# Optimization experiments

Hardware: AMD Instinct MI355X
Metric: run time of the kernel (lower is better)

The kernel has to match this reference:

```python
import jax, jax.numpy as jnp
import numpy as np

N_NODES = 50000
N_EDGES = 800000
IN_FEAT = 128
HIDDEN = 128
HEADS = 4
HEAD_DIM = HIDDEN // HEADS  # 32
N_LAYERS = 3
N_GRAPHS = 64
NEG_SLOPE = 0.2
LN_EPS = 1e-5


def setup_inputs() -> dict:
    key = jax.random.key(0)
    ks = jax.random.split(key, 12)
    x = jax.random.normal(ks[0], (N_NODES, IN_FEAT), dtype=jnp.float32)
    edge_index = jax.random.randint(ks[1], (2, N_EDGES), 0, N_NODES, dtype=jnp.int64)
    batch = jnp.sort(jax.random.randint(ks[2], (N_NODES,), 0, N_GRAPHS, dtype=jnp.int64))
    s = 0.05
    emb_W = jax.random.normal(ks[3], (IN_FEAT, HIDDEN), dtype=jnp.float32) * s
    emb_b = jnp.zeros((HIDDEN,), dtype=jnp.float32)
    lin_l_W = jax.random.normal(ks[4], (N_LAYERS, HIDDEN, HIDDEN), dtype=jnp.float32) * s
    lin_l_b = jnp.zeros((N_LAYERS, HIDDEN), dtype=jnp.float32)
    lin_r_W = jax.random.normal(ks[5], (N_LAYERS, HIDDEN, HIDDEN), dtype=jnp.float32) * s
    lin_r_b = jnp.zeros((N_LAYERS, HIDDEN), dtype=jnp.float32)
    att = jax.random.normal(ks[6], (N_LAYERS, HEADS, HEAD_DIM), dtype=jnp.float32) * s
    conv_b = jnp.zeros((N_LAYERS, HIDDEN), dtype=jnp.float32)
    ln_g = jnp.ones((N_LAYERS, HIDDEN), dtype=jnp.float32)
    ln_b = jnp.zeros((N_LAYERS, HIDDEN), dtype=jnp.float32)
    return {"x": x, "edge_index": edge_index, "batch": batch,
            "emb_W": emb_W, "emb_b": emb_b,
            "lin_l_W": lin_l_W, "lin_l_b": lin_l_b,
            "lin_r_W": lin_r_W, "lin_r_b": lin_r_b,
            "att": att, "conv_b": conv_b, "ln_g": ln_g, "ln_b": ln_b}


def _gatv2_layer(x, src, dst, Wl, bl, Wr, br, att_w, bias):
    # x: [N, HIDDEN]; src/dst: [E]; att_w: [H, C]
    N = x.shape[0]
    xl = (x @ Wl + bl).reshape(N, HEADS, HEAD_DIM)  # source transform
    xr = (x @ Wr + br).reshape(N, HEADS, HEAD_DIM)  # target transform
    e = jax.nn.leaky_relu(xl[src] + xr[dst], NEG_SLOPE)      # [E, H, C]
    logits = jnp.einsum('ehc,hc->eh', e, att_w)              # [E, H]
    # segment softmax over edges grouped by destination node
    seg_max = jax.ops.segment_max(logits, dst, num_segments=N)  # [N, H]
    seg_max = jnp.where(jnp.isfinite(seg_max), seg_max, 0.0)
    ex = jnp.exp(logits - seg_max[dst])
    denom = jax.ops.segment_sum(ex, dst, num_segments=N)
    alpha = ex / (denom[dst] + 1e-16)                        # [E, H]
    msg = alpha[..., None] * xl[src]                         # [E, H, C]
    out = jax.ops.segment_sum(msg, dst, num_segments=N)      # [N, H, C]
    return out.reshape(N, HIDDEN) + bias


def _layer_norm(x, g, b):
    mu = jnp.mean(x, axis=-1, keepdims=True)
    var = jnp.mean(jnp.square(x - mu), axis=-1, keepdims=True)
    return (x - mu) * jax.lax.rsqrt(var + LN_EPS) * g + b


def reference(x, edge_index, batch, emb_W, emb_b, lin_l_W, lin_l_b,
              lin_r_W, lin_r_b, att, conv_b, ln_g, ln_b):
    src, dst = edge_index[0], edge_index[1]
    h = x @ emb_W + emb_b
    for l in range(N_LAYERS):
        res = h
        h = _gatv2_layer(h, src, dst, lin_l_W[l], lin_l_b[l],
                         lin_r_W[l], lin_r_b[l], att[l], conv_b[l])
        h = jax.nn.elu(h)          # dropout in eval mode = identity
        h = h + res
        h = _layer_norm(h, ln_g[l], ln_b[l])
    # global mean pool over graphs
    sums = jax.ops.segment_sum(h, batch, num_segments=N_GRAPHS)
    counts = jax.ops.segment_sum(jnp.ones((h.shape[0], 1), h.dtype), batch,
                                 num_segments=N_GRAPHS)
    return sums / jnp.maximum(counts, 1.0)
```

## Files before the change

### kernel.cpp

```cpp
#include <hip/hip_runtime.h>
#include <hip/hip_bf16.h>
#include <math.h>


#define HID 128
#define BKT_SHIFT 7
#define BKT_DSTS (1 << BKT_SHIFT)
#define CAP_SHIFT 12
#define CAP (1 << CAP_SHIFT)

typedef __attribute__((ext_vector_type(8))) short bf8_t;
typedef __attribute__((ext_vector_type(8))) _Float16 hf8_t;
typedef __attribute__((ext_vector_type(2))) _Float16 h2_t;
typedef __attribute__((ext_vector_type(4))) float f4_t;

__device__ __forceinline__ unsigned short f2bf(float f) {
    unsigned u = __float_as_uint(f);
    u += 0x7fff + ((u >> 16) & 1);
    return (unsigned short)(u >> 16);
}
__device__ __forceinline__ float bf2f(unsigned short h) {
    return __uint_as_float(((unsigned)h) << 16);
}
__device__ __forceinline__ unsigned short f2h(float f) {
    _Float16 h = (_Float16)f;
    return __builtin_bit_cast(unsigned short, h);
}
__device__ __forceinline__ float h2f(unsigned short u) {
    return (float)__builtin_bit_cast(_Float16, u);
}
__device__ __forceinline__ h2_t shfl_xor_h2(h2_t v, int m) {
    return __builtin_bit_cast(h2_t, __shfl_xor(__builtin_bit_cast(int, v), m, 64));
}


__global__ __launch_bounds__(256) void k1_bin_prep(
    const int* __restrict__ ei, int* __restrict__ bucketCursor,
    int* __restrict__ tmp, int E, int NBK, int perBlk,
    const float* __restrict__ embW, const float* __restrict__ linlW,
    const float* __restrict__ linrW, unsigned short* __restrict__ frag) {
    __shared__ int hist[512];
    __shared__ int base[512];
    int tid = threadIdx.x;

    if (blockIdx.x < 256) {
        int e0 = blockIdx.x * perBlk;
        int e1 = e0 + perBlk; if (e1 > E) e1 = E;

        for (int b = tid; b < NBK; b += 256) hist[b] = 0;
        __syncthreads();
        for (int e = e0 + tid; e < e1; e += 256)
            atomicAdd(&hist[ei[E + e] >> BKT_SHIFT], 1);
        __syncthreads();
        for (int b = tid; b < NBK; b += 256) {
            int c = hist[b];
            if (c > 0) base[b] = atomicAdd(&bucketCursor[b], c);
            hist[b] = 0;
        }
        __syncthreads();
        for (int e = e0 + tid; e < e1; e += 256) {
            int d = ei[E + e];
            int b = d >> BKT_SHIFT;
            int pos = (b << CAP_SHIFT) + base[b] + atomicAdd(&hist[b], 1);
            tmp[pos] = ei[e] | ((d & (BKT_DSTS - 1)) << 16);
        }
    } else {
        int bid = blockIdx.x - 256;
        int w = bid >> 6;
        const float* W;
        if (w == 0)      W = embW;
        else if (w <= 3) W = linlW + (size_t)(w - 1) * 16384;
        else             W = linrW + (size_t)(w - 4) * 16384;

        int i = ((bid & 63) << 8) + tid;
        int j = i & 7;
        int lane = (i >> 3) & 63;
        int t = i >> 9;
        int kk = t >> 3, nn = t & 7;
        int k = kk * 32 + (lane >> 4) * 8 + j;
        int n = nn * 16 + (lane & 15);
        float v = W[k * 128 + n];
        if (w == 0) {
            unsigned short hi = f2bf(v);
            frag[i] = hi;
            frag[16384 + i] = f2bf(v - bf2f(hi));
        } else {
            int slot = (w <= 3) ? (1 + 2 * (w - 1)) : (2 + 2 * (w - 4));
            frag[32768 + (size_t)(slot - 1) * 16384 + i] = f2h(v);
        }
    }
}


__global__ __launch_bounds__(256) void k2_bucket_embdual(
    const int* __restrict__ tmp, const int* __restrict__ bucketCursor,
    int* __restrict__ offsets, int* __restrict__ deg,
    unsigned short* __restrict__ srt, int N, int GBLK,
    const float* __restrict__ Afp, const unsigned short* __restrict__ wfrag,
    const float* __restrict__ emb_b,
    const float* __restrict__ bl0, const float* __restrict__ br0,
    unsigned short* __restrict__ Chi, unsigned short* __restrict__ Clo,
    unsigned short* __restrict__ xl, unsigned short* __restrict__ xr) {
    __shared__ __align__(16) unsigned short As[2][64][136];
    int tid = threadIdx.x;

    if (blockIdx.x >= GBLK) {
        int* hist = (int*)As;
        int* cur  = hist + BKT_DSTS;
        int b = blockIdx.x - GBLK;
        int d0 = b << BKT_SHIFT;
        if (tid < BKT_DSTS) hist[tid] = 0;
        __syncthreads();
        int start = b << CAP_SHIFT;
        int end = start + bucketCursor[b];
        for (int i = start + tid; i < end; i += 256)
            atomicAdd(&hist[(tmp[i] >> 16) & (BKT_DSTS - 1)], 1);
        __syncthreads();
        int v = (tid < BKT_DSTS) ? hist[tid] : 0;
        if (tid < BKT_DSTS) cur[tid] = v;
        __syncthreads();
        for (int off = 1; off < BKT_DSTS; off <<= 1) {
            int u = (tid < BKT_DSTS && tid >= off) ? cur[tid - off] : 0;
            __syncthreads();
            if (tid < BKT_DSTS) cur[tid] += u;
            __syncthreads();
        }
        if (tid < BKT_DSTS) {
            int ex = start + cur[tid] - v;
            int d = d0 + tid;
            if (d < N) { offsets[d] = ex; deg[d] = v; }
            cur[tid] = ex;
        }
        __syncthreads();
        for (int i = start + tid; i < end; i += 256) {
            int r = tmp[i];
            int pos = atomicAdd(&cur[(r >> 16) & (BKT_DSTS - 1)], 1);
            srt[pos] = (unsigned short)(r & 0xFFFF);
        }
        return;
    }

    int m0 = blockIdx.x * 64;

    #pragma unroll
    for (int i = 0; i < 8; ++i) {
        int idx = tid + i * 256;
        int r = idx >> 5, c4 = idx & 31;
        int row = m0 + r;
        float4 v = make_float4(0.f, 0.f, 0.f, 0.f);
        if (row < N) v = *(const float4*)(Afp + (size_t)row * HID + c4 * 4);
        ushort4 hi, lo;
        hi.x = f2bf(v.x); lo.x = f2bf(v.x - bf2f(hi.x));
        hi.y = f2bf(v.y); lo.y = f2bf(v.y - bf2f(hi.y));
        hi.z = f2bf(v.z); lo.z = f2bf(v.z - bf2f(hi.z));
        hi.w = f2bf(v.w); lo.w = f2bf(v.w - bf2f(hi.w));
        *(ushort4*)&As[0][r][c4 * 4] = hi;
        *(ushort4*)&As[1][r][c4 * 4] = lo;
    }
    __syncthreads();

    int wave = tid >> 6, lane = tid & 63;
    int mrow = lane & 15;
    int quad = lane >> 4;

    f4_t acc[8];
    #pragma unroll
    for (int nn = 0; nn < 8; ++nn) acc[nn] = (f4_t)(0.f);

    #pragma unroll
    for (int kk = 0; kk < 4; ++kk) {
        bf8_t ah = *(const bf8_t*)&As[0][wave * 16 + mrow][kk * 32 + quad * 8];
        bf8_t al = *(const bf8_t*)&As[1][wave * 16 + mrow][kk * 32 + quad * 8];
        const unsigned short* bp = wfrag + kk * 4096 + lane * 8;
        #pragma unroll
        for (int nn = 0; nn < 8; ++nn) {
            bf8_t bh = *(const bf8_t*)(bp + nn * 512);
            bf8_t bl = *(const bf8_t*)(bp + nn * 512 + 16384);
            acc[nn] = __builtin_amdgcn_mfma_f32_16x16x32_bf16(ah, bh, acc[nn], 0, 0, 0);
            acc[nn] = __builtin_amdgcn_mfma_f32_16x16x32_bf16(ah, bl, acc[nn], 0, 0, 0);
            acc[nn] = __builtin_amdgcn_mfma_f32_16x16x32_bf16(al, bh, acc[nn], 0, 0, 0);
        }
    }

    int lrow0 = wave * 16 + quad * 4;
    __syncthreads();
    #pragma unroll
    for (int nn = 0; nn < 8; ++nn) {
        int col = nn * 16 + mrow;
        float b = emb_b[col];
        #pragma unroll
        for (int r = 0; r < 4; ++r) {
            float o = acc[nn][r] + b;
            unsigned short hh = f2h(o);
            As[0][lrow0 + r][col] = hh;
            As[1][lrow0 + r][col] = f2h(o - h2f(hh));
        }
    }
    __syncthreads();

    hf8_t afr[4];
    #pragma unroll
    for (int kk = 0; kk < 4; ++kk)
        afr[kk] = *(const hf8_t*)&As[0][wave * 16 + mrow][kk * 32 + quad * 8];
    #pragma unroll
    for (int i = 0; i < 4; ++i) {
        int idx = tid + i * 256;
        int r = idx >> 4, c8 = idx & 15;
        int row = m0 + r;
        if (row < N) {
            *(uint4*)(Chi + (size_t)row * HID + c8 * 8) = *(uint4*)&As[0][r][c8 * 8];
            *(uint4*)(Clo + (size_t)row * HID + c8 * 8) = *(uint4*)&As[1][r][c8 * 8];
        }
    }

    f4_t acc0[8], acc1[8];
    #pragma unroll
    for (int nn = 0; nn < 8; ++nn) {
        acc0[nn] = (f4_t)(0.f);
        acc1[nn] = (f4_t)(0.f);
    }
    const unsigned short* Bl = wfrag + 32768;
    const unsigned short* Br = wfrag + 49152;
    #pragma unroll
    for (int kk = 0; kk < 4; ++kk) {
        const unsigned short* bp0 = Bl + kk * 4096 + lane * 8;
        const unsigned short* bp1 = Br + kk * 4096 + lane * 8;
        #pragma unroll
        for (int nn = 0; nn < 8; ++nn) {
            hf8_t bb0 = *(const hf8_t*)(bp0 + nn * 512);
            hf8_t bb1 = *(const hf8_t*)(bp1 + nn * 512);
            acc0[nn] = __builtin_amdgcn_mfma_f32_16x16x32_f16(afr[kk], bb0, acc0[nn], 0, 0, 0);
            acc1[nn] = __builtin_amdgcn_mfma_f32_16x16x32_f16(afr[kk], bb1, acc1[nn], 0, 0, 0);
        }
    }

    __syncthreads();
    #pragma unroll
    for (int nn = 0; nn < 8; ++nn) {
        int col = nn * 16 + mrow;
        float bb0 = bl0[col];
        float bb1 = br0[col];
        #pragma unroll
        for (int r = 0; r < 4; ++r) {
            As[0][lrow0 + r][col] = f2h(acc0[nn][r] + bb0);
            As[1][lrow0 + r][col] = f2h(acc1[nn][r] + bb1);
        }
    }
    __syncthreads();
    #pragma unroll
    for (int i = 0; i < 4; ++i) {
        int idx = tid + i * 256;
        int r = idx >> 4, c8 = idx & 15;
        int row = m0 + r;
        if (row < N) {
            *(uint4*)(xl + (size_t)row * HID + c8 * 8) = *(uint4*)&As[0][r][c8 * 8];
            *(uint4*)(xr + (size_t)row * HID + c8 * 8) = *(uint4*)&As[1][r][c8 * 8];
        }
    }
}


__global__ __launch_bounds__(256) void gemm_dual_f16(
    const unsigned short* __restrict__ Ah,
    const unsigned short* __restrict__ Bf0, const unsigned short* __restrict__ Bf1,
    const float* __restrict__ b0, const float* __restrict__ b1,
    unsigned short* __restrict__ C0h, unsigned short* __restrict__ C1h, int M) {
    __shared__ __align__(16) unsigned short As[2][64][136];
    int m0 = blockIdx.x * 64;
    int tid = threadIdx.x;

    #pragma unroll
    for (int i = 0; i < 4; ++i) {
        int idx = tid + i * 256;
        int r = idx >> 4, c8 = idx & 15;
        int row = m0 + r;
        uint4 v = make_uint4(0, 0, 0, 0);
        if (row < M) v = *(const uint4*)(Ah + (size_t)row * HID + c8 * 8);
        *(uint4*)&As[0][r][c8 * 8] = v;
    }
    __syncthreads();

    int wave = tid >> 6, lane = tid & 63;
    int mrow = lane & 15;
    int quad = lane >> 4;

    f4_t acc0[8], acc1[8];
    #pragma unroll
    for (int nn = 0; nn < 8; ++nn) {
        acc0[nn] = (f4_t)(0.f);
        acc1[nn] = (f4_t)(0.f);
    }

    #pragma unroll
    for (int kk = 0; kk < 4; ++kk) {
        hf8_t a = *(const hf8_t*)&As[0][wave * 16 + mrow][kk * 32 + quad * 8];
        const unsigned short* bp0 = Bf0 + kk * 4096 + lane * 8;
        const unsigned short* bp1 = Bf1 + kk * 4096 + lane * 8;
        #pragma unroll
        for (int nn = 0; nn < 8; ++nn) {
            hf8_t bb0 = *(const hf8_t*)(bp0 + nn * 512);
            hf8_t bb1 = *(const hf8_t*)(bp1 + nn * 512);
            acc0[nn] = __builtin_amdgcn_mfma_f32_16x16x32_f16(a, bb0, acc0[nn], 0, 0, 0);
            acc1[nn] = __builtin_amdgcn_mfma_f32_16x16x32_f16(a, bb1, acc1[nn], 0, 0, 0);
        }
    }

    int lrow0 = wave * 16 + quad * 4;
    __syncthreads();
    #pragma unroll
    for (int nn = 0; nn < 8; ++nn) {
        int col = nn * 16 + mrow;
        float bb0 = b0[col];
        float bb1 = b1[col];
        #pragma unroll
        for (int r = 0; r < 4; ++r) {
            As[0][lrow0 + r][col] = f2h(acc0[nn][r] + bb0);
            As[1][lrow0 + r][col] = f2h(acc1[nn][r] + bb1);
        }
    }
    __syncthreads();
    #pragma unroll
    for (int i = 0; i < 4; ++i) {
        int idx = tid + i * 256;
        int r = idx >> 4, c8 = idx & 15;
        int row = m0 + r;
        if (row < M) {
            *(uint4*)(C0h + (size_t)row * HID + c8 * 8) = *(uint4*)&As[0][r][c8 * 8];
            *(uint4*)(C1h + (size_t)row * HID + c8 * 8) = *(uint4*)&As[1][r][c8 * 8];
        }
    }
}


__device__ __forceinline__ void edge_math(uint4 rv, const h2_t xr2[4], const h2_t av2[4],
                                          h2_t xv[4], float* pOut) {
    const h2_t slope2 = {(_Float16)0.2f, (_Float16)0.2f};
    xv[0] = __builtin_bit_cast(h2_t, rv.x); xv[1] = __builtin_bit_cast(h2_t, rv.y);
    xv[2] = __builtin_bit_cast(h2_t, rv.z); xv[3] = __builtin_bit_cast(h2_t, rv.w);
    h2_t p2 = (h2_t)((_Float16)0.f);
    #pragma unroll
    for (int i = 0; i < 4; ++i) {
        h2_t e = xv[i] + xr2[i];
        e = __builtin_elementwise_max(e, e * slope2);
        p2 = e * av2[i] + p2;
    }
    *pOut = (float)p2[0] + (float)p2[1];
}

__global__ __launch_bounds__(256) void gat_layer(
    const unsigned short* __restrict__ xlh,
    const unsigned short* __restrict__ xrh,
    const int* __restrict__ offsets, const int* __restrict__ deg,
    const unsigned short* __restrict__ srt,
    const float* __restrict__ att,
    const float* __restrict__ convb,
    const float* __restrict__ lng, const float* __restrict__ lnb,
    unsigned short* __restrict__ Hhi, unsigned short* __restrict__ Hlo, int N) {
    int wv = (blockIdx.x * blockDim.x + threadIdx.x) >> 6;
    int lane = threadIdx.x & 63;
    if (wv >= N) return;
    int n = wv;
    int quarter = lane >> 4;
    int f0 = (lane & 15) * 8;
    const unsigned short* xbase = xlh + f0;

    h2_t xr2[4], av2[4];
    {
        uint4 xv = *(const uint4*)(xrh + (size_t)n * HID + f0);
        xr2[0] = __builtin_bit_cast(h2_t, xv.x);
        xr2[1] = __builtin_bit_cast(h2_t, xv.y);
        xr2[2] = __builtin_bit_cast(h2_t, xv.z);
        xr2[3] = __builtin_bit_cast(h2_t, xv.w);
        float a[8];
        *(float4*)&a[0] = *(const float4*)(att + f0);
        *(float4*)&a[4] = *(const float4*)(att + f0 + 4);
        #pragma unroll
        for (int i = 0; i < 4; ++i)
            av2[i] = (h2_t){(_Float16)a[2 * i], (_Float16)a[2 * i + 1]};
    }

    float d = 0.f;
    h2_t acc2[4];
    #pragma unroll
    for (int i = 0; i < 4; ++i) acc2[i] = (h2_t)((_Float16)0.f);
    int start = offsets[n], cnt = deg[n];

    int j = 0;
    for (; j + 16 <= cnt; j += 16) {
        int s[4];
        #pragma unroll
        for (int u = 0; u < 4; ++u) s[u] = srt[start + j + 4 * u + quarter];
        uint4 rv[4];
        #pragma unroll
        for (int u = 0; u < 4; ++u)
            rv[u] = *(const uint4*)(xbase + (size_t)s[u] * HID);
        h2_t xv[4][4];
        float p[4];
        #pragma unroll
        for (int u = 0; u < 4; ++u) edge_math(rv[u], xr2, av2, xv[u], &p[u]);
        h2_t p01 = {(_Float16)p[0], (_Float16)p[1]};
        h2_t p23 = {(_Float16)p[2], (_Float16)p[3]};
        p01 += shfl_xor_h2(p01, 1); p23 += shfl_xor_h2(p23, 1);
        p01 += shfl_xor_h2(p01, 2); p23 += shfl_xor_h2(p23, 2);
        float w[4];
        w[0] = __expf((float)p01[0]); w[1] = __expf((float)p01[1]);
        w[2] = __expf((float)p23[0]); w[3] = __expf((float)p23[1]);
        #pragma unroll
        for (int u = 0; u < 4; ++u) {
            d += w[u];
            h2_t w2 = (h2_t)((_Float16)w[u]);
            #pragma unroll
            for (int i = 0; i < 4; ++i) acc2[i] = w2 * xv[u][i] + acc2[i];
        }
    }
    for (; j + 4 <= cnt; j += 4) {
        int s = srt[start + j + quarter];
        uint4 rv = *(const uint4*)(xbase + (size_t)s * HID);
        h2_t xv[4];
        float p;
        edge_math(rv, xr2, av2, xv, &p);
        p += __shfl_xor(p, 1, 64);
        p += __shfl_xor(p, 2, 64);
        float w = __expf(p);
        d += w;
        h2_t w2 = (h2_t)((_Float16)w);
        #pragma unroll
        for (int i = 0; i < 4; ++i) acc2[i] = w2 * xv[i] + acc2[i];
    }
    if (j < cnt) {
        int r = cnt - j;
        int idx = j + quarter; if (idx > cnt - 1) idx = cnt - 1;
        int s = srt[start + idx];
        uint4 rv = *(const uint4*)(xbase + (size_t)s * HID);
        h2_t xv[4];
        float p;
        edge_math(rv, xr2, av2, xv, &p);
        p += __shfl_xor(p, 1, 64);
        p += __shfl_xor(p, 2, 64);
        float w = (quarter < r) ? __expf(p) : 0.f;
        d += w;
        h2_t w2 = (h2_t)((_Float16)w);
        #pragma unroll
        for (int i = 0; i < 4; ++i) acc2[i] = w2 * xv[i] + acc2[i];
    }

    #pragma unroll
    for (int i = 0; i < 4; ++i) {
        acc2[i] += shfl_xor_h2(acc2[i], 16);
        acc2[i] += shfl_xor_h2(acc2[i], 32);
    }
    d += __shfl_xor(d, 16, 64);
    d += __shfl_xor(d, 32, 64);

    float acc[8];
    #pragma unroll
    for (int i = 0; i < 4; ++i) {
        acc[2 * i]     = (float)acc2[i][0];
        acc[2 * i + 1] = (float)acc2[i][1];
    }

    float inv = 1.f / (d + 1e-16f);
    float t[8];
    {
        float cb[8];
        *(float4*)&cb[0] = *(const float4*)(convb + f0);
        *(float4*)&cb[4] = *(const float4*)(convb + f0 + 4);
        uint4 rh = *(const uint4*)(Hhi + (size_t)n * HID + f0);
        uint4 rl = *(const uint4*)(Hlo + (size_t)n * HID + f0);
        const unsigned short* hs = (const unsigned short*)&rh;
        const unsigned short* ls = (const unsigned short*)&rl;
        #pragma unroll
        for (int i = 0; i < 8; ++i) {
            float g = acc[i] * inv + cb[i];
            g = (g > 0.f) ? g : (__expf(g) - 1.f);
            t[i] = g + (h2f(hs[i]) + h2f(ls[i]));
        }
    }

    float sum = 0.f;
    #pragma unroll
    for (int i = 0; i < 8; ++i) sum += t[i];
    #pragma unroll
    for (int m = 1; m <= 8; m <<= 1) sum += __shfl_xor(sum, m, 64);
    float mu = sum * (1.f / 128.f);
    float q[8], vs = 0.f;
    #pragma unroll
    for (int i = 0; i < 8; ++i) { q[i] = t[i] - mu; vs += q[i] * q[i]; }
    #pragma unroll
    for (int m = 1; m <= 8; m <<= 1) vs += __shfl_xor(vs, m, 64);
    float rstd = rsqrtf(vs * (1.f / 128.f) + 1e-5f);

    if (quarter == 0) {
        float gv[8], bv[8], o[8];
        *(float4*)&gv[0] = *(const float4*)(lng + f0);
        *(float4*)&gv[4] = *(const float4*)(lng + f0 + 4);
        *(float4*)&bv[0] = *(const float4*)(lnb + f0);
        *(float4*)&bv[4] = *(const float4*)(lnb + f0 + 4);
        #pragma unroll
        for (int i = 0; i < 8; ++i) o[i] = q[i] * rstd * gv[i] + bv[i];
        unsigned short hh[8], hl[8];
        #pragma unroll
        for (int i = 0; i < 8; ++i) {
            hh[i] = f2h(o[i]);
            hl[i] = f2h(o[i] - h2f(hh[i]));
        }
        *(uint4*)(Hhi + (size_t)n * HID + f0) = *(uint4*)&hh[0];
        *(uint4*)(Hlo + (size_t)n * HID + f0) = *(uint4*)&hl[0];
    }
}


__global__ __launch_bounds__(256) void pool_partial(const unsigned short* __restrict__ Hhi,
                                                    const unsigned short* __restrict__ Hlo,
                                                    const int* __restrict__ batch,
                                                    float* __restrict__ sums, int N) {
    __shared__ int bsh[64];
    int c0 = blockIdx.x * 64;
    int tid = threadIdx.x;
    if (tid < 64) bsh[tid] = (c0 + tid < N) ? batch[c0 + tid] : -1;
    __syncthreads();

    int r = tid >> 5;
    int f0 = (tid & 31) * 4;
    float4 acc = make_float4(0.f, 0.f, 0.f, 0.f);
    int curg = -1;
    #pragma unroll
    for (int i = 0; i < 8; ++i) {
        int li = r * 8 + i;
        int g = bsh[li];
        if (g < 0) break;
        if (g != curg) {
            if (curg >= 0) {
                atomicAdd(&sums[curg * HID + f0 + 0], acc.x);
                atomicAdd(&sums[curg * HID + f0 + 1], acc.y);
                atomicAdd(&sums[curg * HID + f0 + 2], acc.z);
                atomicAdd(&sums[curg * HID + f0 + 3], acc.w);
            }
            acc = make_float4(0.f, 0.f, 0.f, 0.f);
            curg = g;
        }
        size_t base = (size_t)(c0 + li) * HID + f0;
        ushort4 hh = *(const ushort4*)(Hhi + base);
        ushort4 hl = *(const ushort4*)(Hlo + base);
        acc.x += h2f(hh.x) + h2f(hl.x);
        acc.y += h2f(hh.y) + h2f(hl.y);
        acc.z += h2f(hh.z) + h2f(hl.z);
        acc.w += h2f(hh.w) + h2f(hl.w);
    }
    if (curg >= 0) {
        atomicAdd(&sums[curg * HID + f0 + 0], acc.x);
        atomicAdd(&sums[curg * HID + f0 + 1], acc.y);
        atomicAdd(&sums[curg * HID + f0 + 2], acc.z);
        atomicAdd(&sums[curg * HID + f0 + 3], acc.w);
    }
}

__global__ __launch_bounds__(128) void pool_final(const float* __restrict__ sums,
                                                  const int* __restrict__ batch,
                                                  float* __restrict__ out, int N) {
    int g = blockIdx.x;
    int f = threadIdx.x;
    int lo = 0, hi = N;
    while (lo < hi) { int mid = (lo + hi) >> 1; if (batch[mid] < g) lo = mid + 1; else hi = mid; }
    int s0 = lo;
    lo = 0; hi = N;
    while (lo < hi) { int mid = (lo + hi) >> 1; if (batch[mid] < g + 1) lo = mid + 1; else hi = mid; }
    int cnt = lo - s0; if (cnt < 1) cnt = 1;
    out[g * HID + f] = sums[g * HID + f] / (float)cnt;
}


extern "C" void kernel_launch(void* const* d_in, const int* in_sizes, int n_in,
                              void* d_out, int out_size, void* d_ws, size_t ws_size,
                              hipStream_t stream) {
    const float* x      = (const float*)d_in[0];
    const int*   ei     = (const int*)d_in[1];
    const int*   batch  = (const int*)d_in[2];
    const float* emb_W  = (const float*)d_in[3];
    const float* emb_b  = (const float*)d_in[4];
    const float* linlW  = (const float*)d_in[5];
    const float* linlb  = (const float*)d_in[6];
    const float* linrW  = (const float*)d_in[7];
    const float* linrb  = (const float*)d_in[8];
    const float* att    = (const float*)d_in[9];
    const float* convb  = (const float*)d_in[10];
    const float* lng    = (const float*)d_in[11];
    const float* lnb    = (const float*)d_in[12];
    float* out = (float*)d_out;

    const int N = in_sizes[0] / HID;
    const int E = in_sizes[1] / 2;
    const int NG = out_size / HID;
    const int NBK = (N + BKT_DSTS - 1) / BKT_DSTS;

    char* p = (char*)d_ws;
    unsigned short* xlh = (unsigned short*)p; p += (size_t)N * HID * 2;
    unsigned short* xrh = (unsigned short*)p; p += (size_t)N * HID * 2;
    unsigned short* hhi = (unsigned short*)p; p += (size_t)N * HID * 2;
    unsigned short* hlo = (unsigned short*)p; p += (size_t)N * HID * 2;
    unsigned short* wfrag = (unsigned short*)p; p += (32768 + 6 * 16384) * 2;
    float* sums       = (float*)p; p += (size_t)NG * HID * 4;
    int* bucketCursor = (int*)p; p += (size_t)((NBK + 63) & ~63) * 4;
    int* deg          = (int*)p; p += (size_t)N * 4;
    int* offsets      = (int*)p; p += (size_t)N * 4;
    unsigned short* srt = (unsigned short*)p; p += ((size_t)NBK << CAP_SHIFT) * 2;
    int* tmp          = (int*)p; p += ((size_t)NBK << CAP_SHIFT) * 4;

    size_t zbytes = (size_t)NG * HID * 4 + (size_t)((NBK + 63) & ~63) * 4;
    hipMemsetAsync(sums, 0, zbytes, stream);

    int perBlk = (E + 255) / 256;
    k1_bin_prep<<<256 + 448, 256, 0, stream>>>(ei, bucketCursor, tmp, E, NBK, perBlk,
                                               emb_W, linlW, linrW, wfrag);

    int gblk = (N + 63) / 64;
    k2_bucket_embdual<<<gblk + NBK, 256, 0, stream>>>(tmp, bucketCursor, offsets, deg,
                                                      srt, N, gblk,
                                                      x, wfrag, emb_b, linlb, linrb,
                                                      hhi, hlo, xlh, xrh);

    gat_layer<<<(N + 3) / 4, 256, 0, stream>>>(xlh, xrh, offsets, deg, srt,
                                               att, convb, lng, lnb, hhi, hlo, N);

    for (int l = 1; l < 3; ++l) {
        const unsigned short* wl = wfrag + 32768 + (size_t)(2 * l) * 16384;
        const unsigned short* wr = wfrag + 32768 + (size_t)(2 * l + 1) * 16384;
        gemm_dual_f16<<<gblk, 256, 0, stream>>>(hhi, wl, wr,
                                                linlb + (size_t)l * HID,
                                                linrb + (size_t)l * HID,
                                                xlh, xrh, N);
        gat_layer<<<(N + 3) / 4, 256, 0, stream>>>(xlh, xrh, offsets, deg, srt,
                                                   att + (size_t)l * HID,
                                                   convb + (size_t)l * HID,
                                                   lng + (size_t)l * HID,
                                                   lnb + (size_t)l * HID,
                                                   hhi, hlo, N);
    }

    pool_partial<<<(N + 63) / 64, 256, 0, stream>>>(hhi, hlo, batch, sums, N);
    pool_final<<<NG, 128, 0, stream>>>(sums, batch, out, N);
}
```

Before: 337.3 us.

## Replace bucketed two-pass edge sort with global-atomic count, scan, scatter

Replaces the bucketed counting sort (per-block LDS histograms writing into a packed tmp array, then per-bucket re-sorting) with a direct CSR build. Per-destination degrees are counted with global atomics, each bucket is scanned into offsets, and a new scatter kernel places source indices using per-destination atomic cursors. This drops the intermediate tmp buffer and its extra read/write pass. In exchange it adds a kernel launch, global atomic contention on degree counters, and scattered 2-byte writes, and edge order within a destination becomes nondeterministic.

After: 398.2 us. 1.18x slower.

```diff
diff --git a/kernel.cpp b/kernel.cpp
--- a/kernel.cpp
+++ b/kernel.cpp
@@ -7,7 +7,8 @@
 #define BKT_SHIFT 7
 #define BKT_DSTS (1 << BKT_SHIFT)
 #define CAP_SHIFT 12
-#define CAP (1 << CAP_SHIFT)
+#define CNT_BLOCKS 1024
+#define SCT_BLOCKS 1024
 
 typedef __attribute__((ext_vector_type(8))) short bf8_t;
 typedef __attribute__((ext_vector_type(8))) _Float16 hf8_t;
@@ -34,38 +35,18 @@
 }
 
 
-__global__ __launch_bounds__(256) void k1_bin_prep(
-    const int* __restrict__ ei, int* __restrict__ bucketCursor,
-    int* __restrict__ tmp, int E, int NBK, int perBlk,
+__global__ __launch_bounds__(256) void k1_count_prep(
+    const int* __restrict__ ei, int* __restrict__ deg, int E,
     const float* __restrict__ embW, const float* __restrict__ linlW,
     const float* __restrict__ linrW, unsigned short* __restrict__ frag) {
-    __shared__ int hist[512];
-    __shared__ int base[512];
     int tid = threadIdx.x;
 
-    if (blockIdx.x < 256) {
-        int e0 = blockIdx.x * perBlk;
-        int e1 = e0 + perBlk; if (e1 > E) e1 = E;
-
-        for (int b = tid; b < NBK; b += 256) hist[b] = 0;
-        __syncthreads();
-        for (int e = e0 + tid; e < e1; e += 256)
-            atomicAdd(&hist[ei[E + e] >> BKT_SHIFT], 1);
-        __syncthreads();
-        for (int b = tid; b < NBK; b += 256) {
-            int c = hist[b];
-            if (c > 0) base[b] = atomicAdd(&bucketCursor[b], c);
-            hist[b] = 0;
-        }
-        __syncthreads();
-        for (int e = e0 + tid; e < e1; e += 256) {
-            int d = ei[E + e];
-            int b = d >> BKT_SHIFT;
-            int pos = (b << CAP_SHIFT) + base[b] + atomicAdd(&hist[b], 1);
-            tmp[pos] = ei[e] | ((d & (BKT_DSTS - 1)) << 16);
-        }
+    if (blockIdx.x < CNT_BLOCKS) {
+        int stride = CNT_BLOCKS * 256;
+        for (int e = blockIdx.x * 256 + tid; e < E; e += stride)
+            atomicAdd(&deg[ei[E + e]], 1);
     } else {
-        int bid = blockIdx.x - 256;
+        int bid = blockIdx.x - CNT_BLOCKS;
         int w = bid >> 6;
         const float* W;
         if (w == 0)      W = embW;
@@ -92,10 +73,9 @@
 }
 
 
-__global__ __launch_bounds__(256) void k2_bucket_embdual(
-    const int* __restrict__ tmp, const int* __restrict__ bucketCursor,
-    int* __restrict__ offsets, int* __restrict__ deg,
-    unsigned short* __restrict__ srt, int N, int GBLK,
+__global__ __launch_bounds__(256) void k2_scan_embdual(
+    const int* __restrict__ deg, int* __restrict__ offsets, int* __restrict__ cur,
+    int N, int GBLK,
     const float* __restrict__ Afp, const unsigned short* __restrict__ wfrag,
     const float* __restrict__ emb_b,
     const float* __restrict__ bl0, const float* __restrict__ br0,
@@ -105,37 +85,25 @@
     int tid = threadIdx.x;
 
     if (blockIdx.x >= GBLK) {
-        int* hist = (int*)As;
-        int* cur  = hist + BKT_DSTS;
+        int* sc = (int*)As;
         int b = blockIdx.x - GBLK;
-        int d0 = b << BKT_SHIFT;
-        if (tid < BKT_DSTS) hist[tid] = 0;
-        __syncthreads();
-        int start = b << CAP_SHIFT;
-        int end = start + bucketCursor[b];
-        for (int i = start + tid; i < end; i += 256)
-            atomicAdd(&hist[(tmp[i] >> 16) & (BKT_DSTS - 1)], 1);
-        __syncthreads();
-        int v = (tid < BKT_DSTS) ? hist[tid] : 0;
-        if (tid < BKT_DSTS) cur[tid] = v;
+        int d = (b << BKT_SHIFT) + tid;
+        int v = 0;
+        if (tid < BKT_DSTS) {
+            v = (d < N) ? deg[d] : 0;
+            sc[tid] = v;
+        }
         __syncthreads();
         for (int off = 1; off < BKT_DSTS; off <<= 1) {
-            int u = (tid < BKT_DSTS && tid >= off) ? cur[tid - off] : 0;
+            int u = (tid < BKT_DSTS && tid >= off) ? sc[tid - off] : 0;
             __syncthreads();
-            if (tid < BKT_DSTS) cur[tid] += u;
+            if (tid < BKT_DSTS) sc[tid] += u;
             __syncthreads();
         }
-        if (tid < BKT_DSTS) {
-            int ex = start + cur[tid] - v;
-            int d = d0 + tid;
-            if (d < N) { offsets[d] = ex; deg[d] = v; }
-            cur[tid] = ex;
-        }
-        __syncthreads();
-        for (int i = start + tid; i < end; i += 256) {
-            int r = tmp[i];
-            int pos = atomicAdd(&cur[(r >> 16) & (BKT_DSTS - 1)], 1);
-            srt[pos] = (unsigned short)(r & 0xFFFF);
+        if (tid < BKT_DSTS && d < N) {
+            int o = (b << CAP_SHIFT) + sc[tid] - v;
+            offsets[d] = o;
+            cur[d] = o;
         }
         return;
     }
@@ -256,6 +224,19 @@
             *(uint4*)(xl + (size_t)row * HID + c8 * 8) = *(uint4*)&As[0][r][c8 * 8];
             *(uint4*)(xr + (size_t)row * HID + c8 * 8) = *(uint4*)&As[1][r][c8 * 8];
         }
+    }
+}
+
+
+__global__ __launch_bounds__(256) void k3_scatter(const int* __restrict__ ei,
+                                                  int* __restrict__ cur,
+                                                  unsigned short* __restrict__ srt,
+                                                  int E) {
+    int stride = SCT_BLOCKS * 256;
+    for (int e = blockIdx.x * 256 + threadIdx.x; e < E; e += stride) {
+        int d = ei[E + e];
+        int pos = atomicAdd(&cur[d], 1);
+        srt[pos] = (unsigned short)ei[e];
     }
 }
 
@@ -600,24 +581,23 @@
     unsigned short* hlo = (unsigned short*)p; p += (size_t)N * HID * 2;
     unsigned short* wfrag = (unsigned short*)p; p += (32768 + 6 * 16384) * 2;
     float* sums       = (float*)p; p += (size_t)NG * HID * 4;
-    int* bucketCursor = (int*)p; p += (size_t)((NBK + 63) & ~63) * 4;
     int* deg          = (int*)p; p += (size_t)N * 4;
     int* offsets      = (int*)p; p += (size_t)N * 4;
+    int* cur          = (int*)p; p += (size_t)N * 4;
     unsigned short* srt = (unsigned short*)p; p += ((size_t)NBK << CAP_SHIFT) * 2;
-    int* tmp          = (int*)p; p += ((size_t)NBK << CAP_SHIFT) * 4;
-
-    size_t zbytes = (size_t)NG * HID * 4 + (size_t)((NBK + 63) & ~63) * 4;
+
+    size_t zbytes = (size_t)NG * HID * 4 + (size_t)N * 4;
     hipMemsetAsync(sums, 0, zbytes, stream);
 
-    int perBlk = (E + 255) / 256;
-    k1_bin_prep<<<256 + 448, 256, 0, stream>>>(ei, bucketCursor, tmp, E, NBK, perBlk,
-                                               emb_W, linlW, linrW, wfrag);
+    k1_count_prep<<<CNT_BLOCKS + 448, 256, 0, stream>>>(ei, deg, E,
+                                                        emb_W, linlW, linrW, wfrag);
 
     int gblk = (N + 63) / 64;
-    k2_bucket_embdual<<<gblk + NBK, 256, 0, stream>>>(tmp, bucketCursor, offsets, deg,
-                                                      srt, N, gblk,
-                                                      x, wfrag, emb_b, linlb, linrb,
-                                                      hhi, hlo, xlh, xrh);
+    k2_scan_embdual<<<gblk + NBK, 256, 0, stream>>>(deg, offsets, cur, N, gblk,
+                                                    x, wfrag, emb_b, linlb, linrb,
+                                                    hhi, hlo, xlh, xrh);
+
+    k3_scatter<<<SCT_BLOCKS, 256, 0, stream>>>(ei, cur, srt, E);
 
     gat_layer<<<(N + 3) / 4, 256, 0, stream>>>(xlh, xrh, offsets, deg, srt,
                                                att, convb, lng, lnb, hhi, hlo, N);
```
